# Performance work log

Hardware: AMD Instinct MI355X
Metric: run time of the kernel (lower is better)

Reference implementation:

```python
import jax, jax.numpy as jnp
import numpy as np

N_NODES = 50000
N_EDGES = 512000
D = 128          # node_state_dim
H = 256          # edge hidden / message dim = 2*D (GRU input size)


def _edge_mlp(x, W1, b1, W2, b2):
    # Linear -> ReLU -> Linear, matching nn.Sequential built in build_model
    h = jax.nn.relu(x @ W1.T + b1)
    return h @ W2.T + b2


def _prop_once(node_states, f_idx, t_idx, W1, b1, W2, b2):
    # gather endpoints, concat, edge MLP, scatter-add into destination nodes
    edge_in = jnp.concatenate([node_states[f_idx], node_states[t_idx]], axis=-1)  # [E, 2D]
    msgs = _edge_mlp(edge_in, W1, b1, W2, b2)                                     # [E, H]
    return jax.ops.segment_sum(msgs, t_idx, num_segments=N_NODES)                 # [N, H]


def _gru_cell(x, h, W_ih, W_hh, b_ih, b_hh):
    # PyTorch GRU cell convention
    gi = x @ W_ih.T + b_ih   # [N, 3D]
    gh = h @ W_hh.T + b_hh   # [N, 3D]
    ir, iz, inn = jnp.split(gi, 3, axis=-1)
    hr, hz, hn = jnp.split(gh, 3, axis=-1)
    r = jax.nn.sigmoid(ir + hr)
    z = jax.nn.sigmoid(iz + hz)
    n = jnp.tanh(inn + r * hn)
    return (1.0 - z) * n + z * h


def setup_inputs() -> dict:
    key = jax.random.key(0)
    ks = jax.random.split(key, 16)
    s = 0.1  # edge_net_init_scale-ish small init
    inp = {
        "node_states": jax.random.normal(ks[0], (N_NODES, D), dtype=jnp.float32),
        "from_idx": jax.random.randint(ks[1], (N_EDGES,), 0, N_NODES),
        "to_idx": jax.random.randint(ks[2], (N_EDGES,), 0, N_NODES),
        # forward message net: Linear(2D->H), Linear(H->H)
        "Wf1": jax.random.normal(ks[3], (H, 2 * D), dtype=jnp.float32) * s,
        "bf1": jnp.zeros((H,), jnp.float32),
        "Wf2": jax.random.normal(ks[4], (H, H), dtype=jnp.float32) * s,
        "bf2": jnp.zeros((H,), jnp.float32),
        # reverse message net (separate params)
        "Wr1": jax.random.normal(ks[5], (H, 2 * D), dtype=jnp.float32) * s,
        "br1": jnp.zeros((H,), jnp.float32),
        "Wr2": jax.random.normal(ks[6], (H, H), dtype=jnp.float32) * s,
        "br2": jnp.zeros((H,), jnp.float32),
        # GRU(input=2D, hidden=D) params, torch layout
        "W_ih": jax.random.normal(ks[7], (3 * D, 2 * D), dtype=jnp.float32) * 0.05,
        "W_hh": jax.random.normal(ks[8], (3 * D, D), dtype=jnp.float32) * 0.05,
        "b_ih": jnp.zeros((3 * D,), jnp.float32),
        "b_hh": jnp.zeros((3 * D,), jnp.float32),
    }
    return inp


def reference(node_states, from_idx, to_idx, Wf1, bf1, Wf2, bf2,
              Wr1, br1, Wr2, br2, W_ih, W_hh, b_ih, b_hh):
    agg = _prop_once(node_states, from_idx, to_idx, Wf1, bf1, Wf2, bf2)
    agg = agg + _prop_once(node_states, to_idx, from_idx, Wr1, br1, Wr2, br2)
    return _gru_cell(agg, node_states, W_ih, W_hh, b_ih, b_hh)  # [N, D]
```

## Files before the change

### kernel.cpp

```cpp
#include <hip/hip_runtime.h>
#include <stdint.h>


#define NN 50000
#define NE 512000
#define SCAN_N (2 * NN)
#define SCAN_BLOCKS ((SCAN_N + 1023) / 1024)

typedef unsigned short u16;
typedef unsigned int u32;
using h2  = __attribute__((ext_vector_type(2))) _Float16;
using h4  = __attribute__((ext_vector_type(4))) _Float16;
using h8  = __attribute__((ext_vector_type(8))) _Float16;
using f4v = __attribute__((ext_vector_type(4))) float;

__device__ __forceinline__ float h2f(u16 u) {
  _Float16 h; __builtin_memcpy(&h, &u, 2); return (float)h;
}
__device__ __forceinline__ u16 f2h(float f) {
  _Float16 h = (_Float16)f; u16 u; __builtin_memcpy(&u, &h, 2); return u;
}


__global__ void k_wcat(const float* __restrict__ Wf1, const float* __restrict__ bf1,
                       const float* __restrict__ Wr1, const float* __restrict__ br1,
                       u16* __restrict__ Wc16, float* __restrict__ biascat) {
  int c = blockIdx.x;
  int k = threadIdx.x;
  const float* src;
  if (c < 256)      src = Wf1 + (size_t)c * 256;
  else if (c < 512) src = Wr1 + (size_t)(c - 256) * 256 + 128;
  else if (c < 768) src = Wf1 + (size_t)(c - 512) * 256 + 128;
  else              src = Wr1 + (size_t)(c - 768) * 256;
  float v = src[k];
  int nt = c >> 4, kt = k >> 5, g = (k & 31) >> 3, j = k & 7;
  int lane = (c & 15) + g * 16;
  Wc16[((size_t)nt * 4 + kt) * 512 + lane * 8 + j] = f2h(v);
  if (k == 0) biascat[c] = (c < 256) ? bf1[c] : ((c >= 768) ? br1[c - 768] : 0.f);
}

__global__ void k_gcat(const float* __restrict__ W_ih, const float* __restrict__ Wf2,
                       const float* __restrict__ Wr2, u16* __restrict__ G16) {
  int b = blockIdx.x;
  int c = b % 384, w = b / 384;
  const float* W2 = w ? Wr2 : Wf2;
  int k = threadIdx.x;
  float acc = 0.f;
  for (int o = 0; o < 256; ++o)
    acc = fmaf(W_ih[(size_t)c * 256 + o], W2[(size_t)o * 256 + k], acc);
  int kg = w * 256 + k;
  int nt = c >> 4, kt = kg >> 5, g = (kg & 31) >> 3, j = kg & 7;
  int lane = (c & 15) + g * 16;
  G16[((size_t)nt * 16 + kt) * 512 + lane * 8 + j] = f2h(acc);
}

__global__ void k_whh(const float* __restrict__ W_hh, u16* __restrict__ Wh16) {
  int c = blockIdx.x, k = threadIdx.x;
  float v = W_hh[(size_t)c * 128 + k];
  int nt = c >> 4, kt = k >> 5, g = (k & 31) >> 3, j = k & 7;
  int lane = (c & 15) + g * 16;
  Wh16[((size_t)nt * 4 + kt) * 512 + lane * 8 + j] = f2h(v);
}

__global__ void k_vbias(const float* __restrict__ W_ih, const float* __restrict__ bf2,
                        const float* __restrict__ br2, float* __restrict__ vf,
                        float* __restrict__ vr) {
  int c = blockIdx.x * blockDim.x + threadIdx.x;
  if (c >= 384) return;
  float a = 0.f, b = 0.f;
  for (int o = 0; o < 256; ++o) {
    float w = W_ih[(size_t)c * 256 + o];
    a = fmaf(w, bf2[o], a);
    b = fmaf(w, br2[o], b);
  }
  vf[c] = a; vr[c] = b;
}

__global__ void k_nsh(const float* __restrict__ ns, u16* __restrict__ nsf) {
  int t = blockIdx.x * 256 + threadIdx.x;
  int n = t >> 4, kk8 = t & 15;
  float4 v0 = *(const float4*)(ns + (size_t)n * 128 + kk8 * 8);
  float4 v1 = *(const float4*)(ns + (size_t)n * 128 + kk8 * 8 + 4);
  u16 hv[8] = {f2h(v0.x), f2h(v0.y), f2h(v0.z), f2h(v0.w),
               f2h(v1.x), f2h(v1.y), f2h(v1.z), f2h(v1.w)};
  int mt = n >> 4, r = n & 15, kt = kk8 >> 2, g = kk8 & 3;
  int lane = r + g * 16;
  *(uint4*)(nsf + ((size_t)mt * 4 + kt) * 512 + lane * 8) = *(const uint4*)hv;
}

__global__ void k_hist(const int* __restrict__ from, const int* __restrict__ to,
                       int* __restrict__ cnt) {
  int e = blockIdx.x * 256 + threadIdx.x;
  if (e < NE) {
    atomicAdd(cnt + to[e], 1);
    atomicAdd(cnt + NN + from[e], 1);
  }
}

__global__ __launch_bounds__(256) void k_scanA(const int* __restrict__ cnt,
                                               int* __restrict__ bsum) {
  __shared__ int part[256];
  int b = blockIdx.x, tid = threadIdx.x;
  int idx = b * 1024 + tid * 4;
  int s = 0;
  if (idx + 3 < SCAN_N) {
    int4 v = *(const int4*)(cnt + idx);
    s = v.x + v.y + v.z + v.w;
  } else {
    for (int q = 0; q < 4; ++q)
      if (idx + q < SCAN_N) s += cnt[idx + q];
  }
  part[tid] = s;
  __syncthreads();
  for (int d = 128; d > 0; d >>= 1) {
    if (tid < d) part[tid] += part[tid + d];
    __syncthreads();
  }
  if (tid == 0) bsum[b] = part[0];
}

__global__ __launch_bounds__(128) void k_scanB(int* __restrict__ bsum) {
  __shared__ int part[128];
  int tid = threadIdx.x;
  int v = (tid < SCAN_BLOCKS) ? bsum[tid] : 0;
  part[tid] = v;
  __syncthreads();
  for (int d = 1; d < 128; d <<= 1) {
    int x = (tid >= d) ? part[tid - d] : 0;
    __syncthreads();
    part[tid] += x;
    __syncthreads();
  }
  if (tid < SCAN_BLOCKS) bsum[tid] = (tid > 0) ? part[tid - 1] : 0;
}

__global__ __launch_bounds__(256) void k_scanC(const int* __restrict__ cnt,
                                               const int* __restrict__ bsum,
                                               int* __restrict__ off,
                                               int* __restrict__ cur) {
  __shared__ int part[256];
  int b = blockIdx.x, tid = threadIdx.x;
  int idx = b * 1024 + tid * 4;
  int c[4] = {0, 0, 0, 0};
  if (idx + 3 < SCAN_N) {
    int4 v = *(const int4*)(cnt + idx);
    c[0] = v.x; c[1] = v.y; c[2] = v.z; c[3] = v.w;
  } else {
    for (int q = 0; q < 4; ++q)
      if (idx + q < SCAN_N) c[q] = cnt[idx + q];
  }
  int s = c[0] + c[1] + c[2] + c[3];
  part[tid] = s;
  __syncthreads();
  for (int d = 1; d < 256; d <<= 1) {
    int x = (tid >= d) ? part[tid - d] : 0;
    __syncthreads();
    part[tid] += x;
    __syncthreads();
  }
  int run = bsum[b] + ((tid > 0) ? part[tid - 1] : 0);
#pragma unroll
  for (int q = 0; q < 4; ++q) {
    if (idx + q < SCAN_N) {
      off[idx + q] = run;
      cur[idx + q] = run;
      run += c[q];
    }
  }
  if (b == 0 && tid == 0) off[SCAN_N] = 2 * NE;
}

__global__ void k_fill(const int* __restrict__ from, const int* __restrict__ to,
                       int* __restrict__ cur, int* __restrict__ nbr) {
  int e = blockIdx.x * 256 + threadIdx.x;
  if (e < NE) {
    int f = from[e], t = to[e];
    nbr[atomicAdd(cur + t, 1)] = f;
    nbr[atomicAdd(cur + NN + f, 1)] = t;
  }
}

__global__ __launch_bounds__(256) void k_proj(const u16* __restrict__ nsf,
                                              const u16* __restrict__ Wc16,
                                              const float* __restrict__ biascat,
                                              u16* __restrict__ Tin,
                                              u16* __restrict__ Tnode,
                                              u16* __restrict__ Tout) {
  const int w = threadIdx.x >> 6, lane = threadIdx.x & 63;
  const int mt0 = blockIdx.x * 4;
  const int nt0 = blockIdx.y * 16 + w * 4;
  const h8 hzv = {(_Float16)0.f, (_Float16)0.f, (_Float16)0.f, (_Float16)0.f,
                  (_Float16)0.f, (_Float16)0.f, (_Float16)0.f, (_Float16)0.f};
  f4v acc[4][4];
#pragma unroll
  for (int m = 0; m < 4; ++m)
#pragma unroll
    for (int n = 0; n < 4; ++n) acc[m][n] = (f4v){0.f, 0.f, 0.f, 0.f};

#pragma unroll
  for (int kt = 0; kt < 4; ++kt) {
    h8 a[4], b[4];
#pragma unroll
    for (int m = 0; m < 4; ++m) {
      int mt = mt0 + m;
      a[m] = (mt < 3125) ? *(const h8*)(nsf + ((size_t)mt * 4 + kt) * 512 + lane * 8) : hzv;
    }
#pragma unroll
    for (int n = 0; n < 4; ++n)
      b[n] = *(const h8*)(Wc16 + ((size_t)(nt0 + n) * 4 + kt) * 512 + lane * 8);
#pragma unroll
    for (int m = 0; m < 4; ++m)
#pragma unroll
      for (int n = 0; n < 4; ++n)
        acc[m][n] = __builtin_amdgcn_mfma_f32_16x16x32_f16(a[m], b[n], acc[m][n], 0, 0, 0);
  }

  const int c0 = lane & 15, rB = (lane >> 4) * 4;
#pragma unroll
  for (int n = 0; n < 4; ++n) {
    const int ntg = nt0 + n;
    u16* dst;
    size_t stride;
    int col;
    if (ntg < 16)      { dst = Tin;   stride = 256; col = ntg * 16 + c0; }
    else if (ntg < 48) { dst = Tnode; stride = 512; col = (ntg - 16) * 16 + c0; }
    else               { dst = Tout;  stride = 256; col = (ntg - 48) * 16 + c0; }
    float bias = biascat[ntg * 16 + c0];
#pragma unroll
    for (int m = 0; m < 4; ++m) {
      int mt = mt0 + m;
      if (mt >= 3125) continue;
#pragma unroll
      for (int reg = 0; reg < 4; ++reg) {
        int row = mt * 16 + rB + reg;
        dst[(size_t)row * stride + col] = f2h(acc[m][n][reg] + bias);
      }
    }
  }
}

__global__ __launch_bounds__(256) void k_gather(const u16* __restrict__ Tin,
                                                const u16* __restrict__ Tnode,
                                                const u16* __restrict__ Tout,
                                                const int* __restrict__ nbr,
                                                const int* __restrict__ off,
                                                u16* __restrict__ Sf) {
  const int lane = threadIdx.x & 63;
  const int gid = blockIdx.x * 4 + (threadIdx.x >> 6);
  const int dir = (gid >= NN) ? 1 : 0;
  const int n = gid - dir * NN;
  const int mt = n >> 4, r = n & 15;
  const int g = (lane & 7) >> 1, j0 = (lane & 1) * 4;
  const int laneF = r + g * 16;

  const u16* gtab = dir ? Tout : Tin;
  const int invofs = dir ? 0 : 256;
  const h2 z2 = {(_Float16)0.f, (_Float16)0.f};
  h4 invv = *(const h4*)(Tnode + (size_t)n * 512 + invofs + lane * 4);
  h2 inv01 = {invv[0], invv[1]};
  h2 inv23 = {invv[2], invv[3]};
  const int s = off[dir * NN + n];
  const int e = off[dir * NN + n + 1];
  float a0 = 0.f, a1 = 0.f, a2 = 0.f, a3 = 0.f;

  for (int i = s; i < e; i += 64) {
    int nb = (i + lane < e) ? nbr[i + lane] : 0;
    int cnt = min(64, e - i);
    int k = 0;
    for (; k + 7 < cnt; k += 8) {
      h4 wv[8];
#pragma unroll
      for (int q = 0; q < 8; ++q) {
        int f = __shfl(nb, k + q);
        wv[q] = *(const h4*)(gtab + (size_t)f * 256 + lane * 4);
      }
#pragma unroll
      for (int q = 0; q < 8; ++q) {
        h2 t01 = {wv[q][0], wv[q][1]};
        h2 t23 = {wv[q][2], wv[q][3]};
        t01 = __builtin_elementwise_max(t01 + inv01, z2);
        t23 = __builtin_elementwise_max(t23 + inv23, z2);
        a0 += (float)t01[0]; a1 += (float)t01[1];
        a2 += (float)t23[0]; a3 += (float)t23[1];
      }
    }
    if (k + 3 < cnt) {
      h4 wv[4];
#pragma unroll
      for (int q = 0; q < 4; ++q) {
        int f = __shfl(nb, k + q);
        wv[q] = *(const h4*)(gtab + (size_t)f * 256 + lane * 4);
      }
#pragma unroll
      for (int q = 0; q < 4; ++q) {
        h2 t01 = {wv[q][0], wv[q][1]};
        h2 t23 = {wv[q][2], wv[q][3]};
        t01 = __builtin_elementwise_max(t01 + inv01, z2);
        t23 = __builtin_elementwise_max(t23 + inv23, z2);
        a0 += (float)t01[0]; a1 += (float)t01[1];
        a2 += (float)t23[0]; a3 += (float)t23[1];
      }
      k += 4;
    }
    for (; k < cnt; ++k) {
      int f = __shfl(nb, k);
      h4 wv = *(const h4*)(gtab + (size_t)f * 256 + lane * 4);
      h2 t01 = {wv[0], wv[1]};
      h2 t23 = {wv[2], wv[3]};
      t01 = __builtin_elementwise_max(t01 + inv01, z2);
      t23 = __builtin_elementwise_max(t23 + inv23, z2);
      a0 += (float)t01[0]; a1 += (float)t01[1];
      a2 += (float)t23[0]; a3 += (float)t23[1];
    }
  }
  int kt = dir * 8 + (lane >> 3);
  u16 hv[4] = {f2h(a0), f2h(a1), f2h(a2), f2h(a3)};
  *(ushort4*)(Sf + ((size_t)mt * 16 + kt) * 512 + laneF * 8 + j0) = *(const ushort4*)hv;
}

__global__ __launch_bounds__(256) void k_gru(const u16* __restrict__ Sf,
                                             const u16* __restrict__ nsf,
                                             const u16* __restrict__ G16,
                                             const u16* __restrict__ Wh16,
                                             const float* __restrict__ ns,
                                             const float* __restrict__ b_ih,
                                             const float* __restrict__ b_hh,
                                             const float* __restrict__ vf,
                                             const float* __restrict__ vr,
                                             const int* __restrict__ off,
                                             float* __restrict__ out) {
  const int w = threadIdx.x >> 6, lane = threadIdx.x & 63;
  const int mt0 = (blockIdx.x >> 1) * 2, half = blockIdx.x & 1;
  const int base = half * 4 + w;
  const bool has1 = (mt0 + 1) < 3125;
  const h8 hz = {(_Float16)0.f, (_Float16)0.f, (_Float16)0.f, (_Float16)0.f,
                 (_Float16)0.f, (_Float16)0.f, (_Float16)0.f, (_Float16)0.f};

  f4v gh[2][3], gi[2][3];
#pragma unroll
  for (int m = 0; m < 2; ++m)
#pragma unroll
    for (int g = 0; g < 3; ++g) {
      gh[m][g] = (f4v){0.f, 0.f, 0.f, 0.f};
      gi[m][g] = (f4v){0.f, 0.f, 0.f, 0.f};
    }

#pragma unroll
  for (int kt = 0; kt < 4; ++kt) {
    h8 a0 = *(const h8*)(nsf + ((size_t)mt0 * 4 + kt) * 512 + lane * 8);
    h8 a1 = has1 ? *(const h8*)(nsf + ((size_t)(mt0 + 1) * 4 + kt) * 512 + lane * 8) : hz;
#pragma unroll
    for (int g = 0; g < 3; ++g) {
      h8 b = *(const h8*)(Wh16 + ((size_t)(base + 8 * g) * 4 + kt) * 512 + lane * 8);
      gh[0][g] = __builtin_amdgcn_mfma_f32_16x16x32_f16(a0, b, gh[0][g], 0, 0, 0);
      gh[1][g] = __builtin_amdgcn_mfma_f32_16x16x32_f16(a1, b, gh[1][g], 0, 0, 0);
    }
  }

#pragma unroll
  for (int kt = 0; kt < 16; ++kt) {
    h8 a0 = *(const h8*)(Sf + ((size_t)mt0 * 16 + kt) * 512 + lane * 8);
    h8 a1 = has1 ? *(const h8*)(Sf + ((size_t)(mt0 + 1) * 16 + kt) * 512 + lane * 8) : hz;
#pragma unroll
    for (int g = 0; g < 3; ++g) {
      h8 b = *(const h8*)(G16 + ((size_t)(base + 8 * g) * 16 + kt) * 512 + lane * 8);
      gi[0][g] = __builtin_amdgcn_mfma_f32_16x16x32_f16(a0, b, gi[0][g], 0, 0, 0);
      gi[1][g] = __builtin_amdgcn_mfma_f32_16x16x32_f16(a1, b, gi[1][g], 0, 0, 0);
    }
  }

  const int c0 = lane & 15, rB = (lane >> 4) * 4;
  const int d = base * 16 + c0;
  const float vf0 = vf[d], vf1 = vf[128 + d], vf2 = vf[256 + d];
  const float vr0 = vr[d], vr1 = vr[128 + d], vr2 = vr[256 + d];
  const float bi0 = b_ih[d], bi1 = b_ih[128 + d], bi2 = b_ih[256 + d];
  const float bh0 = b_hh[d], bh1 = b_hh[128 + d], bh2 = b_hh[256 + d];
#pragma unroll
  for (int m = 0; m < 2; ++m) {
    if (m == 1 && !has1) continue;
    const int mt = mt0 + m;
#pragma unroll
    for (int reg = 0; reg < 4; ++reg) {
      int row = mt * 16 + rB + reg;
      float idg = (float)(off[row + 1] - off[row]);
      float odg = (float)(off[NN + row + 1] - off[NN + row]);
      float gr = gi[m][0][reg] + idg * vf0 + odg * vr0 + bi0;
      float gz = gi[m][1][reg] + idg * vf1 + odg * vr1 + bi1;
      float gn = gi[m][2][reg] + idg * vf2 + odg * vr2 + bi2;
      float hr = gh[m][0][reg] + bh0;
      float hzv = gh[m][1][reg] + bh1;
      float hn = gh[m][2][reg] + bh2;
      float rg = 1.f / (1.f + __expf(-(gr + hr)));
      float zg = 1.f / (1.f + __expf(-(gz + hzv)));
      float ng = tanhf(gn + rg * hn);
      float h = ns[(size_t)row * 128 + d];
      out[(size_t)row * 128 + d] = (1.f - zg) * ng + zg * h;
    }
  }
}

extern "C" void kernel_launch(void* const* d_in, const int* in_sizes, int n_in,
                              void* d_out, int out_size, void* d_ws, size_t ws_size,
                              hipStream_t stream) {
  const float* ns   = (const float*)d_in[0];
  const int* from   = (const int*)d_in[1];
  const int* to     = (const int*)d_in[2];
  const float* Wf1  = (const float*)d_in[3];
  const float* bf1  = (const float*)d_in[4];
  const float* Wf2  = (const float*)d_in[5];
  const float* bf2  = (const float*)d_in[6];
  const float* Wr1  = (const float*)d_in[7];
  const float* br1  = (const float*)d_in[8];
  const float* Wr2  = (const float*)d_in[9];
  const float* br2  = (const float*)d_in[10];
  const float* W_ih = (const float*)d_in[11];
  const float* W_hh = (const float*)d_in[12];
  const float* b_ih = (const float*)d_in[13];
  const float* b_hh = (const float*)d_in[14];
  float* out = (float*)d_out;

  char* w = (char*)d_ws;
  u16*   Wc16    = (u16*)(w + 0);
  float* biascat = (float*)(w + 262144);
  u16*   G16     = (u16*)(w + 266240);
  u16*   Wh16    = (u16*)(w + 659456);
  float* vf      = (float*)(w + 757760);
  float* vr      = (float*)(w + 759296);
  int*   cnt     = (int*)(w + 760832);
  int*   off     = (int*)(w + 1160960);
  int*   cur     = (int*)(w + 1561088);
  int*   bsum    = (int*)(w + 1961216);
  int*   nbr     = (int*)(w + 1961728);
  u16*   nsf     = (u16*)(w + 6057728);
  u16*   Tin     = (u16*)(w + 18857728);
  u16*   Tout    = (u16*)(w + 44457728);
  u16*   Tnode   = (u16*)(w + 70057728);
  u16*   Sf      = (u16*)(w + 121257728);

  hipMemsetAsync(cnt, 0, 400000, stream);

  k_wcat<<<1024, 128, 0, stream>>>(Wf1, bf1, Wr1, br1, Wc16, biascat);
  k_gcat<<<768, 256, 0, stream>>>(W_ih, Wf2, Wr2, G16);
  k_whh<<<384, 128, 0, stream>>>(W_hh, Wh16);
  k_vbias<<<3, 128, 0, stream>>>(W_ih, bf2, br2, vf, vr);
  k_nsh<<<3125, 256, 0, stream>>>(ns, nsf);

  k_hist<<<(NE + 255) / 256, 256, 0, stream>>>(from, to, cnt);
  k_scanA<<<SCAN_BLOCKS, 256, 0, stream>>>(cnt, bsum);
  k_scanB<<<1, 128, 0, stream>>>(bsum);
  k_scanC<<<SCAN_BLOCKS, 256, 0, stream>>>(cnt, bsum, off, cur);
  k_fill<<<(NE + 255) / 256, 256, 0, stream>>>(from, to, cur, nbr);

  k_proj<<<dim3(782, 4), 256, 0, stream>>>(nsf, Wc16, biascat, Tin, Tnode, Tout);
  k_gather<<<25000, 256, 0, stream>>>(Tin, Tnode, Tout, nbr, off, Sf);
  k_gru<<<3126, 256, 0, stream>>>(Sf, nsf, G16, Wh16, ns, b_ih, b_hh, vf, vr, off, out);
}
```

Before: 348.2 us.

## Merge prep kernels, fold scanB into scanC, use readlane and nontemporal loads

Five weight and node-state preparation kernels are merged into one launch with block-range dispatch. The separate block-sum scan kernel is removed, and each scanC block now sums the preceding block totals itself from shared memory. The gather loop replaces shfl with readlane for neighbor indices. Nontemporal loads and stores are added in gather and GRU. The aim is to cut launch overhead and cache pollution, at the cost of some redundant per-block prefix work.

```diff
diff --git a/kernel.cpp b/kernel.cpp
--- a/kernel.cpp
+++ b/kernel.cpp
@@ -21,71 +21,72 @@
   _Float16 h = (_Float16)f; u16 u; __builtin_memcpy(&u, &h, 2); return u;
 }
 
-
-__global__ void k_wcat(const float* __restrict__ Wf1, const float* __restrict__ bf1,
-                       const float* __restrict__ Wr1, const float* __restrict__ br1,
-                       u16* __restrict__ Wc16, float* __restrict__ biascat) {
-  int c = blockIdx.x;
-  int k = threadIdx.x;
-  const float* src;
-  if (c < 256)      src = Wf1 + (size_t)c * 256;
-  else if (c < 512) src = Wr1 + (size_t)(c - 256) * 256 + 128;
-  else if (c < 768) src = Wf1 + (size_t)(c - 512) * 256 + 128;
-  else              src = Wr1 + (size_t)(c - 768) * 256;
-  float v = src[k];
-  int nt = c >> 4, kt = k >> 5, g = (k & 31) >> 3, j = k & 7;
-  int lane = (c & 15) + g * 16;
-  Wc16[((size_t)nt * 4 + kt) * 512 + lane * 8 + j] = f2h(v);
-  if (k == 0) biascat[c] = (c < 256) ? bf1[c] : ((c >= 768) ? br1[c - 768] : 0.f);
-}
-
-__global__ void k_gcat(const float* __restrict__ W_ih, const float* __restrict__ Wf2,
-                       const float* __restrict__ Wr2, u16* __restrict__ G16) {
-  int b = blockIdx.x;
-  int c = b % 384, w = b / 384;
-  const float* W2 = w ? Wr2 : Wf2;
-  int k = threadIdx.x;
-  float acc = 0.f;
-  for (int o = 0; o < 256; ++o)
-    acc = fmaf(W_ih[(size_t)c * 256 + o], W2[(size_t)o * 256 + k], acc);
-  int kg = w * 256 + k;
-  int nt = c >> 4, kt = kg >> 5, g = (kg & 31) >> 3, j = kg & 7;
-  int lane = (c & 15) + g * 16;
-  G16[((size_t)nt * 16 + kt) * 512 + lane * 8 + j] = f2h(acc);
-}
-
-__global__ void k_whh(const float* __restrict__ W_hh, u16* __restrict__ Wh16) {
-  int c = blockIdx.x, k = threadIdx.x;
-  float v = W_hh[(size_t)c * 128 + k];
-  int nt = c >> 4, kt = k >> 5, g = (k & 31) >> 3, j = k & 7;
-  int lane = (c & 15) + g * 16;
-  Wh16[((size_t)nt * 4 + kt) * 512 + lane * 8 + j] = f2h(v);
-}
-
-__global__ void k_vbias(const float* __restrict__ W_ih, const float* __restrict__ bf2,
-                        const float* __restrict__ br2, float* __restrict__ vf,
-                        float* __restrict__ vr) {
-  int c = blockIdx.x * blockDim.x + threadIdx.x;
-  if (c >= 384) return;
-  float a = 0.f, b = 0.f;
-  for (int o = 0; o < 256; ++o) {
-    float w = W_ih[(size_t)c * 256 + o];
-    a = fmaf(w, bf2[o], a);
-    b = fmaf(w, br2[o], b);
-  }
-  vf[c] = a; vr[c] = b;
-}
-
-__global__ void k_nsh(const float* __restrict__ ns, u16* __restrict__ nsf) {
-  int t = blockIdx.x * 256 + threadIdx.x;
-  int n = t >> 4, kk8 = t & 15;
-  float4 v0 = *(const float4*)(ns + (size_t)n * 128 + kk8 * 8);
-  float4 v1 = *(const float4*)(ns + (size_t)n * 128 + kk8 * 8 + 4);
-  u16 hv[8] = {f2h(v0.x), f2h(v0.y), f2h(v0.z), f2h(v0.w),
-               f2h(v1.x), f2h(v1.y), f2h(v1.z), f2h(v1.w)};
-  int mt = n >> 4, r = n & 15, kt = kk8 >> 2, g = kk8 & 3;
-  int lane = r + g * 16;
-  *(uint4*)(nsf + ((size_t)mt * 4 + kt) * 512 + lane * 8) = *(const uint4*)hv;
+__global__ __launch_bounds__(256) void k_prep(
+    const float* __restrict__ Wf1, const float* __restrict__ bf1,
+    const float* __restrict__ Wr1, const float* __restrict__ br1,
+    const float* __restrict__ W_ih, const float* __restrict__ Wf2,
+    const float* __restrict__ Wr2, const float* __restrict__ W_hh,
+    const float* __restrict__ bf2, const float* __restrict__ br2,
+    const float* __restrict__ ns,
+    u16* __restrict__ Wc16, float* __restrict__ biascat,
+    u16* __restrict__ G16, u16* __restrict__ Wh16,
+    float* __restrict__ vf, float* __restrict__ vr,
+    u16* __restrict__ nsf) {
+  const int b = blockIdx.x, tid = threadIdx.x;
+  if (b < 512) {
+    int c = b * 2 + (tid >> 7);
+    int k = tid & 127;
+    const float* src;
+    if (c < 256)      src = Wf1 + (size_t)c * 256;
+    else if (c < 512) src = Wr1 + (size_t)(c - 256) * 256 + 128;
+    else if (c < 768) src = Wf1 + (size_t)(c - 512) * 256 + 128;
+    else              src = Wr1 + (size_t)(c - 768) * 256;
+    float v = src[k];
+    int nt = c >> 4, kt = k >> 5, g = (k & 31) >> 3, j = k & 7;
+    int lane = (c & 15) + g * 16;
+    Wc16[((size_t)nt * 4 + kt) * 512 + lane * 8 + j] = f2h(v);
+    if (k == 0) biascat[c] = (c < 256) ? bf1[c] : ((c >= 768) ? br1[c - 768] : 0.f);
+  } else if (b < 1280) {
+    int bb = b - 512;
+    int c = bb % 384, w = bb / 384;
+    const float* W2 = w ? Wr2 : Wf2;
+    int k = tid;
+    float acc = 0.f;
+    for (int o = 0; o < 256; ++o)
+      acc = fmaf(W_ih[(size_t)c * 256 + o], W2[(size_t)o * 256 + k], acc);
+    int kg = w * 256 + k;
+    int nt = c >> 4, kt = kg >> 5, g = (kg & 31) >> 3, j = kg & 7;
+    int lane = (c & 15) + g * 16;
+    G16[((size_t)nt * 16 + kt) * 512 + lane * 8 + j] = f2h(acc);
+  } else if (b < 1472) {
+    int c = (b - 1280) * 2 + (tid >> 7);
+    int k = tid & 127;
+    float v = W_hh[(size_t)c * 128 + k];
+    int nt = c >> 4, kt = k >> 5, g = (k & 31) >> 3, j = k & 7;
+    int lane = (c & 15) + g * 16;
+    Wh16[((size_t)nt * 4 + kt) * 512 + lane * 8 + j] = f2h(v);
+  } else if (b < 1474) {
+    int c = (b - 1472) * 256 + tid;
+    if (c < 384) {
+      float a = 0.f, bb = 0.f;
+      for (int o = 0; o < 256; ++o) {
+        float w = W_ih[(size_t)c * 256 + o];
+        a = fmaf(w, bf2[o], a);
+        bb = fmaf(w, br2[o], bb);
+      }
+      vf[c] = a; vr[c] = bb;
+    }
+  } else {
+    int t = (b - 1474) * 256 + tid;
+    int n = t >> 4, kk8 = t & 15;
+    float4 v0 = *(const float4*)(ns + (size_t)n * 128 + kk8 * 8);
+    float4 v1 = *(const float4*)(ns + (size_t)n * 128 + kk8 * 8 + 4);
+    u16 hv[8] = {f2h(v0.x), f2h(v0.y), f2h(v0.z), f2h(v0.w),
+                 f2h(v1.x), f2h(v1.y), f2h(v1.z), f2h(v1.w)};
+    int mt = n >> 4, r = n & 15, kt = kk8 >> 2, g = kk8 & 3;
+    int lane = r + g * 16;
+    *(uint4*)(nsf + ((size_t)mt * 4 + kt) * 512 + lane * 8) = *(const uint4*)hv;
+  }
 }
 
 __global__ void k_hist(const int* __restrict__ from, const int* __restrict__ to,
@@ -119,27 +120,14 @@
   if (tid == 0) bsum[b] = part[0];
 }
 
-__global__ __launch_bounds__(128) void k_scanB(int* __restrict__ bsum) {
-  __shared__ int part[128];
-  int tid = threadIdx.x;
-  int v = (tid < SCAN_BLOCKS) ? bsum[tid] : 0;
-  part[tid] = v;
-  __syncthreads();
-  for (int d = 1; d < 128; d <<= 1) {
-    int x = (tid >= d) ? part[tid - d] : 0;
-    __syncthreads();
-    part[tid] += x;
-    __syncthreads();
-  }
-  if (tid < SCAN_BLOCKS) bsum[tid] = (tid > 0) ? part[tid - 1] : 0;
-}
-
 __global__ __launch_bounds__(256) void k_scanC(const int* __restrict__ cnt,
                                                const int* __restrict__ bsum,
                                                int* __restrict__ off,
                                                int* __restrict__ cur) {
   __shared__ int part[256];
+  __shared__ int bs[SCAN_BLOCKS];
   int b = blockIdx.x, tid = threadIdx.x;
+  if (tid < SCAN_BLOCKS) bs[tid] = bsum[tid];
   int idx = b * 1024 + tid * 4;
   int c[4] = {0, 0, 0, 0};
   if (idx + 3 < SCAN_N) {
@@ -158,7 +146,9 @@
     part[tid] += x;
     __syncthreads();
   }
-  int run = bsum[b] + ((tid > 0) ? part[tid - 1] : 0);
+  int pre = 0;
+  for (int j = 0; j < b; ++j) pre += bs[j];
+  int run = pre + ((tid > 0) ? part[tid - 1] : 0);
 #pragma unroll
   for (int q = 0; q < 4; ++q) {
     if (idx + q < SCAN_N) {
@@ -256,63 +246,49 @@
   const u16* gtab = dir ? Tout : Tin;
   const int invofs = dir ? 0 : 256;
   const h2 z2 = {(_Float16)0.f, (_Float16)0.f};
-  h4 invv = *(const h4*)(Tnode + (size_t)n * 512 + invofs + lane * 4);
+  h4 invv = __builtin_nontemporal_load(
+      (const h4*)(Tnode + (size_t)n * 512 + invofs + lane * 4));
   h2 inv01 = {invv[0], invv[1]};
   h2 inv23 = {invv[2], invv[3]};
   const int s = off[dir * NN + n];
   const int e = off[dir * NN + n + 1];
   float a0 = 0.f, a1 = 0.f, a2 = 0.f, a3 = 0.f;
 
+#define LOADF(q_, kbase_) \
+  (*(const h4*)(gtab + (size_t)__builtin_amdgcn_readlane(nb, (kbase_) + (q_)) * 256 + lane * 4))
+#define CONSUME(wvq_)                                           \
+  {                                                             \
+    h2 t01 = {(wvq_)[0], (wvq_)[1]};                            \
+    h2 t23 = {(wvq_)[2], (wvq_)[3]};                            \
+    t01 = __builtin_elementwise_max(t01 + inv01, z2);           \
+    t23 = __builtin_elementwise_max(t23 + inv23, z2);           \
+    a0 += (float)t01[0]; a1 += (float)t01[1];                   \
+    a2 += (float)t23[0]; a3 += (float)t23[1];                   \
+  }
+
   for (int i = s; i < e; i += 64) {
-    int nb = (i + lane < e) ? nbr[i + lane] : 0;
+    int nb = (i + lane < e) ? __builtin_nontemporal_load(nbr + i + lane) : 0;
     int cnt = min(64, e - i);
     int k = 0;
     for (; k + 7 < cnt; k += 8) {
-      h4 wv[8];
-#pragma unroll
-      for (int q = 0; q < 8; ++q) {
-        int f = __shfl(nb, k + q);
-        wv[q] = *(const h4*)(gtab + (size_t)f * 256 + lane * 4);
-      }
-#pragma unroll
-      for (int q = 0; q < 8; ++q) {
-        h2 t01 = {wv[q][0], wv[q][1]};
-        h2 t23 = {wv[q][2], wv[q][3]};
-        t01 = __builtin_elementwise_max(t01 + inv01, z2);
-        t23 = __builtin_elementwise_max(t23 + inv23, z2);
-        a0 += (float)t01[0]; a1 += (float)t01[1];
-        a2 += (float)t23[0]; a3 += (float)t23[1];
-      }
+      h4 w0 = LOADF(0, k), w1 = LOADF(1, k), w2 = LOADF(2, k), w3 = LOADF(3, k);
+      h4 w4 = LOADF(4, k), w5 = LOADF(5, k), w6 = LOADF(6, k), w7 = LOADF(7, k);
+      CONSUME(w0) CONSUME(w1) CONSUME(w2) CONSUME(w3)
+      CONSUME(w4) CONSUME(w5) CONSUME(w6) CONSUME(w7)
     }
     if (k + 3 < cnt) {
-      h4 wv[4];
-#pragma unroll
-      for (int q = 0; q < 4; ++q) {
-        int f = __shfl(nb, k + q);
-        wv[q] = *(const h4*)(gtab + (size_t)f * 256 + lane * 4);
-      }
-#pragma unroll
-      for (int q = 0; q < 4; ++q) {
-        h2 t01 = {wv[q][0], wv[q][1]};
-        h2 t23 = {wv[q][2], wv[q][3]};
-        t01 = __builtin_elementwise_max(t01 + inv01, z2);
-        t23 = __builtin_elementwise_max(t23 + inv23, z2);
-        a0 += (float)t01[0]; a1 += (float)t01[1];
-        a2 += (float)t23[0]; a3 += (float)t23[1];
-      }
+      h4 w0 = LOADF(0, k), w1 = LOADF(1, k), w2 = LOADF(2, k), w3 = LOADF(3, k);
+      CONSUME(w0) CONSUME(w1) CONSUME(w2) CONSUME(w3)
       k += 4;
     }
     for (; k < cnt; ++k) {
-      int f = __shfl(nb, k);
-      h4 wv = *(const h4*)(gtab + (size_t)f * 256 + lane * 4);
-      h2 t01 = {wv[0], wv[1]};
-      h2 t23 = {wv[2], wv[3]};
-      t01 = __builtin_elementwise_max(t01 + inv01, z2);
-      t23 = __builtin_elementwise_max(t23 + inv23, z2);
-      a0 += (float)t01[0]; a1 += (float)t01[1];
-      a2 += (float)t23[0]; a3 += (float)t23[1];
-    }
-  }
+      h4 w0 = LOADF(0, k);
+      CONSUME(w0)
+    }
+  }
+#undef LOADF
+#undef CONSUME
+
   int kt = dir * 8 + (lane >> 3);
   u16 hv[4] = {f2h(a0), f2h(a1), f2h(a2), f2h(a3)};
   *(ushort4*)(Sf + ((size_t)mt * 16 + kt) * 512 + laneF * 8 + j0) = *(const ushort4*)hv;
@@ -347,8 +323,10 @@
 
 #pragma unroll
   for (int kt = 0; kt < 4; ++kt) {
-    h8 a0 = *(const h8*)(nsf + ((size_t)mt0 * 4 + kt) * 512 + lane * 8);
-    h8 a1 = has1 ? *(const h8*)(nsf + ((size_t)(mt0 + 1) * 4 + kt) * 512 + lane * 8) : hz;
+    h8 a0 = __builtin_nontemporal_load((const h8*)(nsf + ((size_t)mt0 * 4 + kt) * 512 + lane * 8));
+    h8 a1 = has1 ? __builtin_nontemporal_load(
+                       (const h8*)(nsf + ((size_t)(mt0 + 1) * 4 + kt) * 512 + lane * 8))
+                 : hz;
 #pragma unroll
     for (int g = 0; g < 3; ++g) {
       h8 b = *(const h8*)(Wh16 + ((size_t)(base + 8 * g) * 4 + kt) * 512 + lane * 8);
@@ -359,8 +337,10 @@
 
 #pragma unroll
   for (int kt = 0; kt < 16; ++kt) {
-    h8 a0 = *(const h8*)(Sf + ((size_t)mt0 * 16 + kt) * 512 + lane * 8);
-    h8 a1 = has1 ? *(const h8*)(Sf + ((size_t)(mt0 + 1) * 16 + kt) * 512 + lane * 8) : hz;
+    h8 a0 = __builtin_nontemporal_load((const h8*)(Sf + ((size_t)mt0 * 16 + kt) * 512 + lane * 8));
+    h8 a1 = has1 ? __builtin_nontemporal_load(
+                       (const h8*)(Sf + ((size_t)(mt0 + 1) * 16 + kt) * 512 + lane * 8))
+                 : hz;
 #pragma unroll
     for (int g = 0; g < 3; ++g) {
       h8 b = *(const h8*)(G16 + ((size_t)(base + 8 * g) * 16 + kt) * 512 + lane * 8);
@@ -393,8 +373,8 @@
       float rg = 1.f / (1.f + __expf(-(gr + hr)));
       float zg = 1.f / (1.f + __expf(-(gz + hzv)));
       float ng = tanhf(gn + rg * hn);
-      float h = ns[(size_t)row * 128 + d];
-      out[(size_t)row * 128 + d] = (1.f - zg) * ng + zg * h;
+      float h = __builtin_nontemporal_load(ns + (size_t)row * 128 + d);
+      __builtin_nontemporal_store((1.f - zg) * ng + zg * h, out + (size_t)row * 128 + d);
     }
   }
 }
@@ -439,15 +419,11 @@
 
   hipMemsetAsync(cnt, 0, 400000, stream);
 
-  k_wcat<<<1024, 128, 0, stream>>>(Wf1, bf1, Wr1, br1, Wc16, biascat);
-  k_gcat<<<768, 256, 0, stream>>>(W_ih, Wf2, Wr2, G16);
-  k_whh<<<384, 128, 0, stream>>>(W_hh, Wh16);
-  k_vbias<<<3, 128, 0, stream>>>(W_ih, bf2, br2, vf, vr);
-  k_nsh<<<3125, 256, 0, stream>>>(ns, nsf);
+  k_prep<<<4599, 256, 0, stream>>>(Wf1, bf1, Wr1, br1, W_ih, Wf2, Wr2, W_hh,
+                                   bf2, br2, ns, Wc16, biascat, G16, Wh16, vf, vr, nsf);
 
   k_hist<<<(NE + 255) / 256, 256, 0, stream>>>(from, to, cnt);
   k_scanA<<<SCAN_BLOCKS, 256, 0, stream>>>(cnt, bsum);
-  k_scanB<<<1, 128, 0, stream>>>(bsum);
   k_scanC<<<SCAN_BLOCKS, 256, 0, stream>>>(cnt, bsum, off, cur);
   k_fill<<<(NE + 255) / 256, 256, 0, stream>>>(from, to, cur, nbr);
 
```

Measured after the change: 386.5 us. 11.0% more time.
